# Kernel tuning notes

Hardware: AMD Instinct MI355X
Metric: run time of the kernel (lower is better)

Reference implementation:

```python
import jax, jax.numpy as jnp
import numpy as np

D = 1024   # model dim (hard-coded in ClsNet)
H = 16     # num_heads
HD = D // H
FF = 2048  # torch TransformerEncoderLayer default dim_feedforward
B, LX, LY = 8, 512, 512
EPS = 1e-5
NEG = -1e9


def setup_inputs() -> dict:
    key = jax.random.key(0)
    ks = jax.random.split(key, 16)
    s = 0.02
    inp = {
        "x": jax.random.normal(ks[0], (B, LX, D), jnp.float32),
        "y": jax.random.normal(ks[1], (B, LY, D), jnp.float32),
        "cls": jax.random.normal(ks[2], (D,), jnp.float32) * s,
        "sep": jax.random.normal(ks[3], (D,), jnp.float32) * s,
        "px": jax.random.normal(ks[4], (D,), jnp.float32) * s,
        "py": jax.random.normal(ks[5], (D,), jnp.float32) * s,
        "Wqkv": jax.random.normal(ks[6], (3 * D, D), jnp.float32) * s,
        "bqkv": jnp.zeros((3 * D,), jnp.float32),
        "Wo": jax.random.normal(ks[7], (D, D), jnp.float32) * s,
        "bo": jnp.zeros((D,), jnp.float32),
        "W1": jax.random.normal(ks[8], (FF, D), jnp.float32) * s,
        "b1": jnp.zeros((FF,), jnp.float32),
        "W2": jax.random.normal(ks[9], (D, FF), jnp.float32) * s,
        "b2": jnp.zeros((D,), jnp.float32),
        "ln1_g": jnp.ones((D,), jnp.float32),
        "ln1_b": jnp.zeros((D,), jnp.float32),
        "ln2_g": jnp.ones((D,), jnp.float32),
        "ln2_b": jnp.zeros((D,), jnp.float32),
        "x_len": jax.random.randint(ks[10], (B,), 1, LX + 1, jnp.int32),
        "y_len": jax.random.randint(ks[11], (B,), 1, LY + 1, jnp.int32),
    }
    return inp


def _merge(x, y, cls, sep, px, py, x_len, y_len):
    # Vectorized version of ClsNet.merge: [CLS] x_i+px ... [SEP] y_i+py ... [SEP] pad...
    Bn, Lx, Dd = x.shape
    Ly = y.shape[1]
    S = Lx + Ly + 3
    pos = jnp.arange(S)[None, :]            # [1,S]
    lx = x_len[:, None]                     # [B,1]
    ly = y_len[:, None]
    is_cls = pos == 0                       # [1,S]
    is_x = (pos >= 1) & (pos <= lx)         # [B,S]
    is_sep1 = pos == lx + 1
    is_y = (pos >= lx + 2) & (pos <= lx + ly + 1)
    is_sep2 = pos == lx + ly + 2
    xi = jnp.clip(pos - 1, 0, Lx - 1)       # [1,S]
    yi = jnp.clip(pos - lx - 2, 0, Ly - 1)  # [B,S]
    xg = jnp.take_along_axis(x, xi[:, :, None], axis=1)  # [B,S,D] (broadcast batch)
    yg = jnp.take_along_axis(y, yi[:, :, None], axis=1)  # [B,S,D]
    seq = (jnp.where(is_x[..., None], xg + px, 0.0)
           + jnp.where(is_y[..., None], yg + py, 0.0)
           + is_cls[..., None] * cls
           + (is_sep1 | is_sep2)[..., None] * sep)       # [B,S,D]
    mask = is_cls | is_x | is_sep1 | is_y | is_sep2      # [B,S] True = valid token
    return seq, mask


def _ln(h, g, b):
    m = jnp.mean(h, axis=-1, keepdims=True)
    v = jnp.mean(jnp.square(h - m), axis=-1, keepdims=True)
    return (h - m) * jax.lax.rsqrt(v + EPS) * g + b


def _encoder_layer(seq, mask, Wqkv, bqkv, Wo, bo, W1, b1, W2, b2, ln1_g, ln1_b, ln2_g, ln2_b):
    Bn, S, Dd = seq.shape
    qkv = seq @ Wqkv.T + bqkv                              # [B,S,3D]
    q, k, v = jnp.split(qkv, 3, axis=-1)
    q = q.reshape(Bn, S, H, HD)
    k = k.reshape(Bn, S, H, HD)
    v = v.reshape(Bn, S, H, HD)
    bias = jnp.where(mask, 0.0, NEG)[:, None, None, :]     # padded KEYS masked out
    scores = jnp.einsum("bqhd,bkhd->bhqk", q, k) / np.sqrt(HD) + bias
    attn = jax.nn.softmax(scores, axis=-1)
    o = jnp.einsum("bhqk,bkhd->bqhd", attn, v).reshape(Bn, S, Dd)
    o = o @ Wo.T + bo
    h = _ln(seq + o, ln1_g, ln1_b)                          # post-norm (torch default)
    f = jax.nn.relu(h @ W1.T + b1) @ W2.T + b2
    return _ln(h + f, ln2_g, ln2_b)


def reference(x, y, cls, sep, px, py, Wqkv, bqkv, Wo, bo, W1, b1, W2, b2,
              ln1_g, ln1_b, ln2_g, ln2_b, x_len, y_len):
    seq, mask = _merge(x, y, cls, sep, px, py, x_len, y_len)
    out = _encoder_layer(seq, mask, Wqkv, bqkv, Wo, bo, W1, b1, W2, b2,
                         ln1_g, ln1_b, ln2_g, ln2_b)
    # torch code returns a[0] of the seq-first tensor -> the CLS position for all batches
    return out[:, 0, :]
```

## Files before the change

### kernel.cpp

```cpp
#include <hip/hip_runtime.h>
#include <hip/hip_bf16.h>

#define D_ 1024
#define H_ 16
#define FF_ 2048
#define B_ 8
#define S_ 1027
#define MPAD_ 8320
#define PSTR_ 1088
#define EPS_ 1e-5f

typedef __hip_bfloat16 bf16;
typedef unsigned short u16;
typedef unsigned int u32;
typedef __attribute__((ext_vector_type(4))) float floatx4;
typedef __bf16 bf16x8 __attribute__((ext_vector_type(8)));

__device__ __forceinline__ float2 bfpair(u32 u) {
  union { u32 u; float f; } lo, hi;
  lo.u = u << 16; hi.u = u & 0xffff0000u;
  return make_float2(lo.f, hi.f);
}

__device__ __forceinline__ u32 f2bfbits(float f) {
  union { bf16 h; u16 u; } cv; cv.h = __float2bfloat16(f); return (u32)cv.u;
}

__device__ __forceinline__ float block_sum(float x, float* red) {
  const int t = threadIdx.x;
  __syncthreads();
  red[t] = x;
  __syncthreads();
  for (int s = 128; s > 0; s >>= 1) {
    if (t < s) red[t] += red[t + s];
    __syncthreads();
  }
  return red[0];
}

__device__ __forceinline__ float block_max(float x, float* red) {
  const int t = threadIdx.x;
  __syncthreads();
  red[t] = x;
  __syncthreads();
  for (int s = 128; s > 0; s >>= 1) {
    if (t < s) red[t] = fmaxf(red[t], red[t + s]);
    __syncthreads();
  }
  return red[0];
}

__device__ __forceinline__ void merge_src(
    int b, int s, int lx, int ly,
    const float* __restrict__ x, const float* __restrict__ y,
    const float* __restrict__ cls, const float* __restrict__ sep,
    const float* __restrict__ px, const float* __restrict__ py,
    const float*& src, const float*& add) {
  src = nullptr; add = nullptr;
  if (s == 0) src = cls;
  else if (s <= lx) { src = x + ((size_t)b * 512 + (s - 1)) * D_; add = px; }
  else if (s == lx + 1) src = sep;
  else if (s <= lx + ly + 1) { src = y + ((size_t)b * 512 + (s - lx - 2)) * D_; add = py; }
  else if (s == lx + ly + 2) src = sep;
}

__global__ void __launch_bounds__(256) qr_kernel(
    const float* __restrict__ cls, const float* __restrict__ Wqkv,
    const float* __restrict__ bqkv, u16* __restrict__ RT_hi,
    u16* __restrict__ RT_lo) {
  const int cc = blockIdx.x, h = blockIdx.y, t = threadIdx.x;
  __shared__ float clds[D_];
  __shared__ float qs[64];
  *(float4*)&clds[t * 4] = ((const float4*)cls)[t];
  __syncthreads();
  const int w = t >> 6, l = t & 63;
#pragma unroll 2
  for (int e8 = 0; e8 < 16; ++e8) {
    const int e = e8 * 4 + w;
    const float4* wr = (const float4*)(Wqkv + (size_t)(h * 64 + e) * D_) + l;
    float acc = 0.f;
#pragma unroll
    for (int c = 0; c < 4; ++c) {
      float4 wv = wr[c * 64];
      const float* cp = &clds[c * 256 + l * 4];
      acc += wv.x * cp[0] + wv.y * cp[1] + wv.z * cp[2] + wv.w * cp[3];
    }
#pragma unroll
    for (int off = 32; off > 0; off >>= 1) acc += __shfl_down(acc, off, 64);
    if (l == 0) qs[e] = (acc + bqkv[h * 64 + e]) * 0.125f;
  }
  __syncthreads();
  const int c = cc * 256 + t;
  const float* Wk = Wqkv + (size_t)(D_ + h * 64) * D_ + c;
  float acc = 0.f;
#pragma unroll 8
  for (int e = 0; e < 64; ++e) acc += Wk[(size_t)e * D_] * qs[e];
  const u32 hb = f2bfbits(acc);
  union { u32 u; float f; } hv; hv.u = hb << 16;
  RT_hi[h * D_ + c] = (u16)hb;
  RT_lo[h * D_ + c] = (u16)f2bfbits(acc - hv.f);
}

__global__ void __launch_bounds__(256) scores_kernel(
    const float* __restrict__ x, const float* __restrict__ y,
    const float* __restrict__ cls, const float* __restrict__ sep,
    const float* __restrict__ px, const float* __restrict__ py,
    const int* __restrict__ x_len, const int* __restrict__ y_len,
    const u16* __restrict__ RT_hi, const u16* __restrict__ RT_lo,
    float* __restrict__ S) {
  const int m0 = blockIdx.x * 64;
  bool anyvalid = false;
#pragma unroll
  for (int b = 0; b < B_; ++b) {
    int rs = b * S_, re = rs + x_len[b] + y_len[b] + 3;
    if (m0 < re && m0 + 64 > rs) anyvalid = true;
  }
  if (!anyvalid) return;
  const int t = threadIdx.x;
  const int w = t >> 6, lane = t & 63, lane16 = lane & 15, quad = lane >> 4;
  const int row = m0 + w * 16 + lane16;
  const int b = row / S_;
  const int s = row - b * S_;
  const float* src = nullptr;
  const float* add = nullptr;
  if (b < B_) merge_src(b, s, x_len[b], y_len[b], x, y, cls, sep, px, py, src, add);
  const u16* bh = RT_hi + lane16 * D_ + quad * 8;
  const u16* bl = RT_lo + lane16 * D_ + quad * 8;
  floatx4 acc = {};
#pragma unroll 4
  for (int kt = 0; kt < 32; ++kt) {
    const int col = kt * 32 + quad * 8;
    union { bf16x8 v; u16 u[8]; } au;
    if (src) {
      float4 a0 = *(const float4*)(src + col);
      float4 a1 = *(const float4*)(src + col + 4);
      if (add) {
        float4 p0 = *(const float4*)(add + col);
        float4 p1 = *(const float4*)(add + col + 4);
        a0.x += p0.x; a0.y += p0.y; a0.z += p0.z; a0.w += p0.w;
        a1.x += p1.x; a1.y += p1.y; a1.z += p1.z; a1.w += p1.w;
      }
      au.u[0] = (u16)f2bfbits(a0.x); au.u[1] = (u16)f2bfbits(a0.y);
      au.u[2] = (u16)f2bfbits(a0.z); au.u[3] = (u16)f2bfbits(a0.w);
      au.u[4] = (u16)f2bfbits(a1.x); au.u[5] = (u16)f2bfbits(a1.y);
      au.u[6] = (u16)f2bfbits(a1.z); au.u[7] = (u16)f2bfbits(a1.w);
    } else {
#pragma unroll
      for (int j = 0; j < 8; ++j) au.u[j] = 0;
    }
    bf16x8 vh = *(const bf16x8*)(bh + kt * 32);
    bf16x8 vl = *(const bf16x8*)(bl + kt * 32);
    acc = __builtin_amdgcn_mfma_f32_16x16x32_bf16(au.v, vh, acc, 0, 0, 0);
    acc = __builtin_amdgcn_mfma_f32_16x16x32_bf16(au.v, vl, acc, 0, 0, 0);
  }
  *(floatx4*)&S[(size_t)lane16 * MPAD_ + m0 + w * 16 + quad * 4] = acc;
}

__global__ void __launch_bounds__(256) softmax_kernel(
    const float* __restrict__ S, const int* __restrict__ x_len,
    const int* __restrict__ y_len, u16* __restrict__ P) {
  const int h = blockIdx.x, b = blockIdx.y, t = threadIdx.x;
  const int n = x_len[b] + y_len[b] + 3;
  __shared__ float sc[PSTR_];
  __shared__ float red[256];
  const float* Sp = S + (size_t)h * MPAD_ + b * S_;
  float lmax = -3.0e38f;
  for (int k = t; k < n; k += 256) {
    float s = Sp[k];
    sc[k] = s;
    lmax = fmaxf(lmax, s);
  }
  const float gmax = block_max(lmax, red);
  float lsum = 0.f;
  for (int k = t; k < n; k += 256) {
    float p = __expf(sc[k] - gmax);
    sc[k] = p;
    lsum += p;
  }
  const float inv = 1.0f / block_sum(lsum, red);
  u16* Pp = P + (size_t)(h * 8 + b) * PSTR_;
  for (int k = t; k < PSTR_; k += 256)
    Pp[k] = (k < n) ? (u16)f2bfbits(sc[k] * inv) : (u16)0;
}

__global__ void __launch_bounds__(256) cbar_kernel(
    const float* __restrict__ x, const float* __restrict__ y,
    const float* __restrict__ cls, const float* __restrict__ sep,
    const float* __restrict__ px, const float* __restrict__ py,
    const int* __restrict__ x_len, const int* __restrict__ y_len,
    const u16* __restrict__ P, float* __restrict__ cbar) {
  const int ct = blockIdx.x, b = blockIdx.y, t = threadIdx.x;
  const int c0 = ct * 64;
  const int lx = x_len[b], ly = y_len[b];
  const int n = lx + ly + 3;
  const int nkt = (n + 63) >> 6;
  __shared__ u16 tile[64 * 70];
  const int w = t >> 6, lane = t & 63, lane16 = lane & 15, quad = lane >> 4;
  const int r = t >> 2;
  const int g = (t & 3) * 16;
  const u16* Pp = P + (size_t)(lane16 * 8 + b) * PSTR_;
  floatx4 acc = {};
  for (int kt = 0; kt < nkt; ++kt) {
    const int k0 = kt * 64;
    __syncthreads();
    const int gk = k0 + r;
    u32 packed[8] = {};
    if (gk < n) {
      const float* src; const float* add;
      merge_src(b, gk, lx, ly, x, y, cls, sep, px, py, src, add);
      const float* sp = src + c0 + g;
#pragma unroll
      for (int q = 0; q < 4; ++q) {
        float4 v = *(const float4*)(sp + q * 4);
        if (add) {
          float4 a = *(const float4*)(add + c0 + g + q * 4);
          v.x += a.x; v.y += a.y; v.z += a.z; v.w += a.w;
        }
        packed[q * 2]     = f2bfbits(v.x) | (f2bfbits(v.y) << 16);
        packed[q * 2 + 1] = f2bfbits(v.z) | (f2bfbits(v.w) << 16);
      }
    }
#pragma unroll
    for (int q = 0; q < 8; ++q)
      *(u32*)&tile[r * 70 + g + q * 2] = packed[q];
    __syncthreads();
#pragma unroll
    for (int half = 0; half < 2; ++half) {
      const int kk = half * 32;
      bf16x8 a = *(const bf16x8*)(Pp + k0 + kk + quad * 8);
      union { bf16x8 v; u16 u[8]; } bu;
#pragma unroll
      for (int j = 0; j < 8; ++j)
        bu.u[j] = tile[(kk + quad * 8 + j) * 70 + w * 16 + lane16];
      acc = __builtin_amdgcn_mfma_f32_16x16x32_bf16(a, bu.v, acc, 0, 0, 0);
    }
  }
#pragma unroll
  for (int r4 = 0; r4 < 4; ++r4)
    cbar[(size_t)(b * 16 + quad * 4 + r4) * D_ + c0 + w * 16 + lane16] = acc[r4];
}

template <int K, int N, int BSTR, bool INBF, bool OUTBF, bool RELU, bool PERHEAD>
__global__ void __launch_bounds__(256) gemv8_kernel(
    const void* __restrict__ in_, const float* __restrict__ W,
    const float* __restrict__ bias, void* __restrict__ out_) {
  const int t = threadIdx.x;
  const int hoff = PERHEAD ? ((blockIdx.x * 4) >> 6) * D_ : 0;
  __shared__ u16 lsb[INBF ? 8 * K : 1];
  __shared__ float lsf[INBF ? 1 : 8 * K];
  if (INBF) {
    const u16* in = (const u16*)in_;
    const int per = 8 * K / (256 * 8);
#pragma unroll
    for (int i = 0; i < per; ++i) {
      int flat = (t + i * 256) * 8;
      int b = flat / K, k = flat % K;
      *(uint4*)&lsb[flat] = *(const uint4*)(in + (size_t)b * BSTR + hoff + k);
    }
  } else {
    const float* in = (const float*)in_;
    const int per = 8 * K / (256 * 4);
#pragma unroll
    for (int i = 0; i < per; ++i) {
      int flat = (t + i * 256) * 4;
      int b = flat / K, k = flat % K;
      *(float4*)&lsf[flat] = *(const float4*)(in + (size_t)b * BSTR + hoff + k);
    }
  }
  __syncthreads();
  const int w = t >> 6, l = t & 63;
  const int r = blockIdx.x * 4 + w;
  float acc[8] = {};
#pragma unroll
  for (int ch = 0; ch < K / 256; ++ch) {
    float4 wv = *(const float4*)(W + (size_t)r * K + ch * 256 + l * 4);
#pragma unroll
    for (int b = 0; b < 8; ++b) {
      float i0, i1, i2, i3;
      if (INBF) {
        uint2 u = *(const uint2*)&lsb[b * K + ch * 256 + l * 4];
        float2 p0 = bfpair(u.x), p1 = bfpair(u.y);
        i0 = p0.x; i1 = p0.y; i2 = p1.x; i3 = p1.y;
      } else {
        const float* p = &lsf[b * K + ch * 256 + l * 4];
        i0 = p[0]; i1 = p[1]; i2 = p[2]; i3 = p[3];
      }
      acc[b] += wv.x * i0 + wv.y * i1 + wv.z * i2 + wv.w * i3;
    }
  }
#pragma unroll
  for (int off = 32; off > 0; off >>= 1)
#pragma unroll
    for (int b = 0; b < 8; ++b) acc[b] += __shfl_down(acc[b], off, 64);
  if (l == 0) {
    const float bs = bias[r];
#pragma unroll
    for (int b = 0; b < 8; ++b) {
      float v = acc[b] + bs;
      if (RELU) v = fmaxf(v, 0.f);
      if (OUTBF) ((bf16*)out_)[(size_t)b * N + r] = __float2bfloat16(v);
      else       ((float*)out_)[(size_t)b * N + r] = v;
    }
  }
}

__global__ void __launch_bounds__(256) w1ln_kernel(
    const float* __restrict__ att, const float* __restrict__ cls,
    const float* __restrict__ g1, const float* __restrict__ be1,
    const float* __restrict__ W1, const float* __restrict__ b1,
    bf16* __restrict__ f1) {
  const int t = threadIdx.x;
  __shared__ float ls[8 * D_];
  __shared__ float mn[8], rsd[8];
  float4 cv = ((const float4*)cls)[t];
#pragma unroll
  for (int i = 0; i < 8; ++i) {
    float4 a = ((const float4*)(att + (size_t)i * D_))[t];
    a.x += cv.x; a.y += cv.y; a.z += cv.z; a.w += cv.w;
    *(float4*)&ls[i * D_ + t * 4] = a;
  }
  __syncthreads();
  {
    const int b = t >> 5, j = t & 31;
    const float* base = &ls[b * D_ + j * 32];
    float s = 0.f, s2 = 0.f;
#pragma unroll
    for (int k = 0; k < 32; ++k) { float v = base[k]; s += v; s2 += v * v; }
#pragma unroll
    for (int off = 16; off > 0; off >>= 1) {
      s += __shfl_down(s, off, 32);
      s2 += __shfl_down(s2, off, 32);
    }
    if (j == 0) {
      float mean = s * (1.f / D_);
      mn[b] = mean;
      rsd[b] = rsqrtf(s2 * (1.f / D_) - mean * mean + EPS_);
    }
  }
  __syncthreads();
  {
    const int b = t >> 5, j = t & 31;
    const float mean = mn[b], rs = rsd[b];
    float* base = &ls[b * D_ + j * 32];
    const float* gp = &g1[j * 32];
    const float* bp = &be1[j * 32];
#pragma unroll
    for (int k = 0; k < 32; ++k)
      base[k] = (base[k] - mean) * rs * gp[k] + bp[k];
  }
  __syncthreads();
  const int w = t >> 6, l = t & 63;
  const int r = blockIdx.x * 4 + w;
  float acc[8] = {};
#pragma unroll
  for (int ch = 0; ch < 4; ++ch) {
    float4 wv = *(const float4*)(W1 + (size_t)r * D_ + ch * 256 + l * 4);
#pragma unroll
    for (int b = 0; b < 8; ++b) {
      const float* p = &ls[b * D_ + ch * 256 + l * 4];
      acc[b] += wv.x * p[0] + wv.y * p[1] + wv.z * p[2] + wv.w * p[3];
    }
  }
#pragma unroll
  for (int off = 32; off > 0; off >>= 1)
#pragma unroll
    for (int b = 0; b < 8; ++b) acc[b] += __shfl_down(acc[b], off, 64);
  if (l == 0) {
    const float bs = b1[r];
#pragma unroll
    for (int b = 0; b < 8; ++b)
      f1[(size_t)b * FF_ + r] = __float2bfloat16(fmaxf(acc[b] + bs, 0.f));
  }
}

__global__ void __launch_bounds__(256) ln2_kernel(
    const float* __restrict__ cls, const float* __restrict__ att,
    const float* __restrict__ f2, const float* __restrict__ g1,
    const float* __restrict__ be1, const float* __restrict__ g2,
    const float* __restrict__ be2, float* __restrict__ out) {
  const int b = blockIdx.x, t = threadIdx.x;
  __shared__ float v[D_];
  __shared__ float red[256];
  for (int i = t; i < D_; i += 256) v[i] = cls[i] + att[(size_t)b * D_ + i];
  __syncthreads();
  float ls = 0.f;
  for (int i = t; i < D_; i += 256) ls += v[i];
  const float m1 = block_sum(ls, red) * (1.f / D_);
  float lv = 0.f;
  for (int i = t; i < D_; i += 256) { float dk = v[i] - m1; lv += dk * dk; }
  const float rs1 = rsqrtf(block_sum(lv, red) * (1.f / D_) + EPS_);
  __syncthreads();
  for (int i = t; i < D_; i += 256)
    v[i] = (v[i] - m1) * rs1 * g1[i] + be1[i] + f2[(size_t)b * D_ + i];
  __syncthreads();
  float ls2 = 0.f;
  for (int i = t; i < D_; i += 256) ls2 += v[i];
  const float m2 = block_sum(ls2, red) * (1.f / D_);
  float lv2 = 0.f;
  for (int i = t; i < D_; i += 256) { float dk = v[i] - m2; lv2 += dk * dk; }
  const float rs2 = rsqrtf(block_sum(lv2, red) * (1.f / D_) + EPS_);
  for (int i = t; i < D_; i += 256)
    out[(size_t)b * D_ + i] = (v[i] - m2) * rs2 * g2[i] + be2[i];
}

extern "C" void kernel_launch(void* const* d_in, const int* in_sizes, int n_in,
                              void* d_out, int out_size, void* d_ws, size_t ws_size,
                              hipStream_t stream) {
  (void)in_sizes; (void)n_in; (void)out_size; (void)ws_size;
  const float* x    = (const float*)d_in[0];
  const float* y    = (const float*)d_in[1];
  const float* cls  = (const float*)d_in[2];
  const float* sep  = (const float*)d_in[3];
  const float* px   = (const float*)d_in[4];
  const float* py   = (const float*)d_in[5];
  const float* Wqkv = (const float*)d_in[6];
  const float* bqkv = (const float*)d_in[7];
  const float* Wo   = (const float*)d_in[8];
  const float* bo   = (const float*)d_in[9];
  const float* W1   = (const float*)d_in[10];
  const float* b1   = (const float*)d_in[11];
  const float* W2   = (const float*)d_in[12];
  const float* b2   = (const float*)d_in[13];
  const float* g1   = (const float*)d_in[14];
  const float* be1  = (const float*)d_in[15];
  const float* g2   = (const float*)d_in[16];
  const float* be2  = (const float*)d_in[17];
  const int* xl     = (const int*)d_in[18];
  const int* yl     = (const int*)d_in[19];

  char* ws = (char*)d_ws;
  u16*   RT_hi = (u16*)(ws);
  u16*   RT_lo = (u16*)(ws + 32768);
  float* S     = (float*)(ws + 65536);
  u16*   P     = (u16*)(ws + 598016);
  float* cbar  = (float*)(ws + 876544);
  float* o0    = (float*)(ws + 1400832);
  float* att   = (float*)(ws + 1433600);
  bf16*  f1    = (bf16*)(ws + 1466368);
  float* f2    = (float*)(ws + 1499136);

  qr_kernel<<<dim3(4, 16), 256, 0, stream>>>(cls, Wqkv, bqkv, RT_hi, RT_lo);
  scores_kernel<<<130, 256, 0, stream>>>(x, y, cls, sep, px, py, xl, yl,
                                         RT_hi, RT_lo, S);
  softmax_kernel<<<dim3(16, 8), 256, 0, stream>>>(S, xl, yl, P);
  cbar_kernel<<<dim3(16, 8), 256, 0, stream>>>(x, y, cls, sep, px, py, xl, yl,
                                               P, cbar);
  gemv8_kernel<1024, 1024, 16384, false, false, false, true>
      <<<256, 256, 0, stream>>>(cbar, Wqkv + (size_t)2048 * 1024, bqkv + 2048, o0);
  gemv8_kernel<1024, 1024, 1024, false, false, false, false>
      <<<256, 256, 0, stream>>>(o0, Wo, bo, att);
  w1ln_kernel<<<512, 256, 0, stream>>>(att, cls, g1, be1, W1, b1, f1);
  gemv8_kernel<2048, 1024, 2048, true, false, false, false>
      <<<256, 256, 0, stream>>>(f1, W2, b2, f2);
  ln2_kernel<<<B_, 256, 0, stream>>>(cls, att, f2, g1, be1, g2, be2,
                                     (float*)d_out);
}
```

Baseline: 230.7 us.

## Materialize merged sequence in bf16 once and reuse in scores and cbar

Adds a build_seq kernel that gathers the CLS/x/SEP/y tokens, adds the position vectors and writes one bf16 copy of the merged sequence to workspace. The scores and cbar kernels then read these bf16 rows directly, with no per-element merge logic, fp32 loads or conversions in their inner loops. The cbar kernel also switches to 32-wide K tiles with a smaller shared tile, and the P stride shrinks to match. In exchange there is an extra launch plus a 17 MB intermediate write and two reads of it. Padded rows are left unwritten and are only consumed in masked positions.

After: 205.9 us. 10.7% less time.

```diff
diff --git a/kernel.cpp b/kernel.cpp
--- a/kernel.cpp
+++ b/kernel.cpp
@@ -7,7 +7,7 @@
 #define B_ 8
 #define S_ 1027
 #define MPAD_ 8320
-#define PSTR_ 1088
+#define PSTR_ 1056
 #define EPS_ 1e-5f
 
 typedef __hip_bfloat16 bf16;
@@ -50,18 +50,34 @@
   return red[0];
 }
 
-__device__ __forceinline__ void merge_src(
-    int b, int s, int lx, int ly,
+__global__ void __launch_bounds__(256) build_seq_kernel(
     const float* __restrict__ x, const float* __restrict__ y,
     const float* __restrict__ cls, const float* __restrict__ sep,
     const float* __restrict__ px, const float* __restrict__ py,
-    const float*& src, const float*& add) {
-  src = nullptr; add = nullptr;
+    const int* __restrict__ x_len, const int* __restrict__ y_len,
+    bf16* __restrict__ seq) {
+  const int m = blockIdx.x, t = threadIdx.x;
+  const int b = m / S_;
+  const int s = m - b * S_;
+  if (b >= B_) return;
+  const float* src = nullptr;
+  const float* add = nullptr;
+  const int lx = x_len[b], ly = y_len[b];
   if (s == 0) src = cls;
   else if (s <= lx) { src = x + ((size_t)b * 512 + (s - 1)) * D_; add = px; }
   else if (s == lx + 1) src = sep;
   else if (s <= lx + ly + 1) { src = y + ((size_t)b * 512 + (s - lx - 2)) * D_; add = py; }
   else if (s == lx + ly + 2) src = sep;
+  if (!src) return;
+  float4 sv = ((const float4*)src)[t];
+  if (add) {
+    float4 av = ((const float4*)add)[t];
+    sv.x += av.x; sv.y += av.y; sv.z += av.z; sv.w += av.w;
+  }
+  uint2 o;
+  o.x = f2bfbits(sv.x) | (f2bfbits(sv.y) << 16);
+  o.y = f2bfbits(sv.z) | (f2bfbits(sv.w) << 16);
+  ((uint2*)(seq + (size_t)m * D_))[t] = o;
 }
 
 __global__ void __launch_bounds__(256) qr_kernel(
@@ -102,56 +118,31 @@
 }
 
 __global__ void __launch_bounds__(256) scores_kernel(
-    const float* __restrict__ x, const float* __restrict__ y,
-    const float* __restrict__ cls, const float* __restrict__ sep,
-    const float* __restrict__ px, const float* __restrict__ py,
-    const int* __restrict__ x_len, const int* __restrict__ y_len,
-    const u16* __restrict__ RT_hi, const u16* __restrict__ RT_lo,
-    float* __restrict__ S) {
+    const bf16* __restrict__ seq, const u16* __restrict__ RT_hi,
+    const u16* __restrict__ RT_lo, const int* __restrict__ x_len,
+    const int* __restrict__ y_len, float* __restrict__ S) {
   const int m0 = blockIdx.x * 64;
-  bool anyvalid = false;
+  bool valid = false;
 #pragma unroll
   for (int b = 0; b < B_; ++b) {
     int rs = b * S_, re = rs + x_len[b] + y_len[b] + 3;
-    if (m0 < re && m0 + 64 > rs) anyvalid = true;
-  }
-  if (!anyvalid) return;
+    if (m0 < re && m0 + 64 > rs) valid = true;
+  }
+  if (!valid) return;
   const int t = threadIdx.x;
   const int w = t >> 6, lane = t & 63, lane16 = lane & 15, quad = lane >> 4;
   const int row = m0 + w * 16 + lane16;
-  const int b = row / S_;
-  const int s = row - b * S_;
-  const float* src = nullptr;
-  const float* add = nullptr;
-  if (b < B_) merge_src(b, s, x_len[b], y_len[b], x, y, cls, sep, px, py, src, add);
+  const u16* arow = (const u16*)seq + (size_t)row * D_ + quad * 8;
   const u16* bh = RT_hi + lane16 * D_ + quad * 8;
   const u16* bl = RT_lo + lane16 * D_ + quad * 8;
   floatx4 acc = {};
-#pragma unroll 4
+#pragma unroll
   for (int kt = 0; kt < 32; ++kt) {
-    const int col = kt * 32 + quad * 8;
-    union { bf16x8 v; u16 u[8]; } au;
-    if (src) {
-      float4 a0 = *(const float4*)(src + col);
-      float4 a1 = *(const float4*)(src + col + 4);
-      if (add) {
-        float4 p0 = *(const float4*)(add + col);
-        float4 p1 = *(const float4*)(add + col + 4);
-        a0.x += p0.x; a0.y += p0.y; a0.z += p0.z; a0.w += p0.w;
-        a1.x += p1.x; a1.y += p1.y; a1.z += p1.z; a1.w += p1.w;
-      }
-      au.u[0] = (u16)f2bfbits(a0.x); au.u[1] = (u16)f2bfbits(a0.y);
-      au.u[2] = (u16)f2bfbits(a0.z); au.u[3] = (u16)f2bfbits(a0.w);
-      au.u[4] = (u16)f2bfbits(a1.x); au.u[5] = (u16)f2bfbits(a1.y);
-      au.u[6] = (u16)f2bfbits(a1.z); au.u[7] = (u16)f2bfbits(a1.w);
-    } else {
-#pragma unroll
-      for (int j = 0; j < 8; ++j) au.u[j] = 0;
-    }
+    bf16x8 a  = *(const bf16x8*)(arow + kt * 32);
     bf16x8 vh = *(const bf16x8*)(bh + kt * 32);
     bf16x8 vl = *(const bf16x8*)(bl + kt * 32);
-    acc = __builtin_amdgcn_mfma_f32_16x16x32_bf16(au.v, vh, acc, 0, 0, 0);
-    acc = __builtin_amdgcn_mfma_f32_16x16x32_bf16(au.v, vl, acc, 0, 0, 0);
+    acc = __builtin_amdgcn_mfma_f32_16x16x32_bf16(a, vh, acc, 0, 0, 0);
+    acc = __builtin_amdgcn_mfma_f32_16x16x32_bf16(a, vl, acc, 0, 0, 0);
   }
   *(floatx4*)&S[(size_t)lane16 * MPAD_ + m0 + w * 16 + quad * 4] = acc;
 }
@@ -184,60 +175,36 @@
 }
 
 __global__ void __launch_bounds__(256) cbar_kernel(
-    const float* __restrict__ x, const float* __restrict__ y,
-    const float* __restrict__ cls, const float* __restrict__ sep,
-    const float* __restrict__ px, const float* __restrict__ py,
+    const bf16* __restrict__ seq, const u16* __restrict__ P,
     const int* __restrict__ x_len, const int* __restrict__ y_len,
-    const u16* __restrict__ P, float* __restrict__ cbar) {
+    float* __restrict__ cbar) {
   const int ct = blockIdx.x, b = blockIdx.y, t = threadIdx.x;
   const int c0 = ct * 64;
-  const int lx = x_len[b], ly = y_len[b];
-  const int n = lx + ly + 3;
-  const int nkt = (n + 63) >> 6;
-  __shared__ u16 tile[64 * 70];
+  const int n = x_len[b] + y_len[b] + 3;
+  const int nkt = (n + 31) >> 5;
+  __shared__ u16 tile[32 * 68];
   const int w = t >> 6, lane = t & 63, lane16 = lane & 15, quad = lane >> 4;
-  const int r = t >> 2;
-  const int g = (t & 3) * 16;
-  const u16* Pp = P + (size_t)(lane16 * 8 + b) * PSTR_;
+  const int sk = t >> 3, scg = (t & 7) * 8;
   floatx4 acc = {};
   for (int kt = 0; kt < nkt; ++kt) {
-    const int k0 = kt * 64;
+    const int k0 = kt * 32;
     __syncthreads();
-    const int gk = k0 + r;
-    u32 packed[8] = {};
-    if (gk < n) {
-      const float* src; const float* add;
-      merge_src(b, gk, lx, ly, x, y, cls, sep, px, py, src, add);
-      const float* sp = src + c0 + g;
-#pragma unroll
-      for (int q = 0; q < 4; ++q) {
-        float4 v = *(const float4*)(sp + q * 4);
-        if (add) {
-          float4 a = *(const float4*)(add + c0 + g + q * 4);
-          v.x += a.x; v.y += a.y; v.z += a.z; v.w += a.w;
-        }
-        packed[q * 2]     = f2bfbits(v.x) | (f2bfbits(v.y) << 16);
-        packed[q * 2 + 1] = f2bfbits(v.z) | (f2bfbits(v.w) << 16);
-      }
-    }
-#pragma unroll
-    for (int q = 0; q < 8; ++q)
-      *(u32*)&tile[r * 70 + g + q * 2] = packed[q];
+    uint4 v = make_uint4(0u, 0u, 0u, 0u);
+    if (k0 + sk < n)
+      v = *(const uint4*)((const u16*)seq + (size_t)(b * S_ + k0 + sk) * D_ + c0 + scg);
+    *(uint2*)&tile[sk * 68 + scg]     = make_uint2(v.x, v.y);
+    *(uint2*)&tile[sk * 68 + scg + 4] = make_uint2(v.z, v.w);
     __syncthreads();
-#pragma unroll
-    for (int half = 0; half < 2; ++half) {
-      const int kk = half * 32;
-      bf16x8 a = *(const bf16x8*)(Pp + k0 + kk + quad * 8);
-      union { bf16x8 v; u16 u[8]; } bu;
-#pragma unroll
-      for (int j = 0; j < 8; ++j)
-        bu.u[j] = tile[(kk + quad * 8 + j) * 70 + w * 16 + lane16];
-      acc = __builtin_amdgcn_mfma_f32_16x16x32_bf16(a, bu.v, acc, 0, 0, 0);
-    }
-  }
-#pragma unroll
-  for (int r4 = 0; r4 < 4; ++r4)
-    cbar[(size_t)(b * 16 + quad * 4 + r4) * D_ + c0 + w * 16 + lane16] = acc[r4];
+    bf16x8 a = *(const bf16x8*)(P + (size_t)(lane16 * 8 + b) * PSTR_ + k0 + quad * 8);
+    union { bf16x8 v; u16 u[8]; } bu;
+#pragma unroll
+    for (int j = 0; j < 8; ++j)
+      bu.u[j] = tile[(quad * 8 + j) * 68 + w * 16 + lane16];
+    acc = __builtin_amdgcn_mfma_f32_16x16x32_bf16(a, bu.v, acc, 0, 0, 0);
+  }
+#pragma unroll
+  for (int r = 0; r < 4; ++r)
+    cbar[(size_t)(b * 16 + quad * 4 + r) * D_ + c0 + w * 16 + lane16] = acc[r];
 }
 
 template <int K, int N, int BSTR, bool INBF, bool OUTBF, bool RELU, bool PERHEAD>
@@ -429,22 +396,22 @@
   const int* yl     = (const int*)d_in[19];
 
   char* ws = (char*)d_ws;
-  u16*   RT_hi = (u16*)(ws);
-  u16*   RT_lo = (u16*)(ws + 32768);
-  float* S     = (float*)(ws + 65536);
-  u16*   P     = (u16*)(ws + 598016);
-  float* cbar  = (float*)(ws + 876544);
-  float* o0    = (float*)(ws + 1400832);
-  float* att   = (float*)(ws + 1433600);
-  bf16*  f1    = (bf16*)(ws + 1466368);
-  float* f2    = (float*)(ws + 1499136);
-
+  bf16*  seq   = (bf16*)(ws);
+  u16*   RT_hi = (u16*)(ws + 17039360);
+  u16*   RT_lo = (u16*)(ws + 17072128);
+  float* S     = (float*)(ws + 17104896);
+  u16*   P     = (u16*)(ws + 17637376);
+  float* cbar  = (float*)(ws + 17907712);
+  float* o0    = (float*)(ws + 18432000);
+  float* att   = (float*)(ws + 18464768);
+  bf16*  f1    = (bf16*)(ws + 18497536);
+  float* f2    = (float*)(ws + 18530304);
+
+  build_seq_kernel<<<MPAD_, 256, 0, stream>>>(x, y, cls, sep, px, py, xl, yl, seq);
   qr_kernel<<<dim3(4, 16), 256, 0, stream>>>(cls, Wqkv, bqkv, RT_hi, RT_lo);
-  scores_kernel<<<130, 256, 0, stream>>>(x, y, cls, sep, px, py, xl, yl,
-                                         RT_hi, RT_lo, S);
+  scores_kernel<<<130, 256, 0, stream>>>(seq, RT_hi, RT_lo, xl, yl, S);
   softmax_kernel<<<dim3(16, 8), 256, 0, stream>>>(S, xl, yl, P);
-  cbar_kernel<<<dim3(16, 8), 256, 0, stream>>>(x, y, cls, sep, px, py, xl, yl,
-                                               P, cbar);
+  cbar_kernel<<<dim3(16, 8), 256, 0, stream>>>(seq, P, xl, yl, cbar);
   gemv8_kernel<1024, 1024, 16384, false, false, false, true>
       <<<256, 256, 0, stream>>>(cbar, Wqkv + (size_t)2048 * 1024, bqkv + 2048, o0);
   gemv8_kernel<1024, 1024, 1024, false, false, false, false>
```
